# Performance work log

Hardware: AMD Instinct MI355X
Metric: run time of the kernel (lower is better)

Reference implementation:

```python
import jax, jax.numpy as jnp
import numpy as np

V, E, U, B, S = 32000, 512, 1024, 16, 128
BN_EPS = 1e-3  # keras BatchNormalization default


def setup_inputs() -> dict:
    key = jax.random.key(0)
    ks = jax.random.split(key, 12)
    w = 0.05  # small init keeps the relu-activated LSTM recurrence stable
    return {
        "inputs": jax.random.randint(ks[0], (B, S), 0, V),
        "enc_hidden": jax.random.normal(ks[1], (B, U), jnp.float32) * 0.1,
        "enc_cell": jax.random.normal(ks[2], (B, U), jnp.float32) * 0.1,
        "emb": jax.random.normal(ks[3], (V, E), jnp.float32) * w,
        "Wx": jax.random.normal(ks[4], (E, 4 * U), jnp.float32) * w,
        "Wh": jax.random.normal(ks[5], (U, 4 * U), jnp.float32) * w,
        "b": jnp.zeros((4 * U,), jnp.float32),
        "gamma": jnp.ones((U,), jnp.float32),
        "beta": jnp.zeros((U,), jnp.float32),
        "mov_mean": jnp.zeros((U,), jnp.float32),
        "mov_var": jnp.ones((U,), jnp.float32),
        "W1": jax.random.normal(ks[6], (U, U), jnp.float32) * w,
        "b1": jnp.zeros((U,), jnp.float32),
        "W2": jax.random.normal(ks[7], (U, V), jnp.float32) * w,
        "b2": jnp.zeros((V,), jnp.float32),
    }


def _lstm_relu(xg, mask, h0, c0, Wh):
    # xg: [S,B,4U] precomputed input gates; mask: [S,B] (mask_zero semantics)
    def step(carry, inp):
        h, c = carry
        g, m = inp
        z = g + h @ Wh  # [B,4U]
        i, f, cc, o = jnp.split(z, 4, axis=-1)  # keras gate order i,f,c,o
        i = jax.nn.sigmoid(i)
        f = jax.nn.sigmoid(f)
        o = jax.nn.sigmoid(o)
        cc = jax.nn.relu(cc)  # activation='relu' on candidate
        c_new = f * c + i * cc
        h_new = o * jax.nn.relu(c_new)  # activation='relu' on output
        m = m[:, None]
        h_new = jnp.where(m, h_new, h)  # masked step: carry state/output
        c_new = jnp.where(m, c_new, c)
        return (h_new, c_new), h_new

    (_, _), hs = jax.lax.scan(step, (h0, c0), (xg, mask))
    return hs  # [S,B,U]


def reference(inputs, enc_hidden, enc_cell, emb, Wx, Wh, b, gamma, beta,
              mov_mean, mov_var, W1, b1, W2, b2):
    x = emb[inputs]                       # [B,S,E]
    mask = (inputs != 0)                  # mask_zero=True
    xg = jnp.einsum("bse,eg->bsg", x, Wx) + b   # [B,S,4U]
    hs = _lstm_relu(xg.transpose(1, 0, 2), mask.T, enc_hidden, enc_cell, Wh)
    h = hs.transpose(1, 0, 2)             # [B,S,U]
    # BatchNorm (inference: moving statistics), Dropout is identity at inference
    hbn = (h - mov_mean) * jax.lax.rsqrt(mov_var + BN_EPS) * gamma + beta
    d1 = jax.nn.relu(hbn @ W1 + b1)       # [B,S,U]
    logits = d1 @ W2 + b2                 # [B,S,V]
    return jax.nn.softmax(logits, axis=-1)
```

## Files before the change

kernel.cpp:

```cpp
#include <hip/hip_runtime.h>
#include <hip/hip_bf16.h>
#include <stdint.h>

typedef unsigned short u16;
typedef unsigned int u32;
typedef unsigned long long u64;
typedef __attribute__((ext_vector_type(4))) float f32x4;
typedef __attribute__((ext_vector_type(8))) short s16x8;
typedef __attribute__((ext_vector_type(4))) unsigned int u32x4;

#define AT_LD(p)    __hip_atomic_load((p), __ATOMIC_RELAXED, __HIP_MEMORY_SCOPE_AGENT)
#define AT_ST(p, v) __hip_atomic_store((p), (v), __ATOMIC_RELAXED, __HIP_MEMORY_SCOPE_AGENT)
#define AT_FAA(p)   __hip_atomic_fetch_add((p), 1u, __ATOMIC_RELAXED, __HIP_MEMORY_SCOPE_AGENT)


static __device__ __forceinline__ u16 f2bf(float f) {
  union { float f; unsigned u; } v; v.f = f;
  unsigned r = v.u + 0x7FFFu + ((v.u >> 16) & 1u);
  return (u16)(r >> 16);
}

static __device__ __forceinline__ float bf2f(u16 b) {
  union { unsigned u; float f; } v; v.u = ((u32)b) << 16;
  return v.f;
}

static __device__ __forceinline__ void gload_lds16(const void* g, void* l) {
  __builtin_amdgcn_global_load_lds(
      (const __attribute__((address_space(1))) unsigned int*)(uintptr_t)g,
      (__attribute__((address_space(3))) unsigned int*)(uintptr_t)l,
      16, 0, 0);
}

static __device__ __forceinline__ int swzB(int B) {
  int pos = (B >> 4) & 127;
  int row = (B >> 11) & 15;
  int slot = (pos ^ row ^ (pos >> 3)) & 7;
  int npos = (pos & 0x78) | slot;
  return (B & ~0x7F0) | (npos << 4);
}


__global__ void embed_kernel(const int* __restrict__ inputs,
                             const float* __restrict__ emb,
                             u16* __restrict__ xbf) {
  int i = blockIdx.x * 256 + threadIdx.x;
  int row = i >> 6;
  int e0 = (i & 63) << 3;
  int tok = inputs[row];
  const float* src = emb + (size_t)tok * 512 + e0;
  s16x8 o;
#pragma unroll
  for (int j = 0; j < 8; ++j) o[j] = (short)f2bf(src[j]);
  *(s16x8*)(xbf + (size_t)row * 512 + e0) = o;
}

__global__ void mask_kernel(const int* __restrict__ inputs, u64* __restrict__ mb) {
  int t = threadIdx.x;
  if (t < 32) {
    int b = t >> 1, h = t & 1;
    u64 m = 0;
    for (int j = 0; j < 64; ++j)
      m |= (u64)(inputs[b * 128 + h * 64 + j] != 0) << j;
    mb[t] = m;
  }
}

__global__ void transpose_bf16(const float* __restrict__ W, u16* __restrict__ Wt,
                               int K, int N) {
  __shared__ float t[32][33];
  int ntn = N >> 5;
  int tn = blockIdx.x % ntn, tk = blockIdx.x / ntn;
  int n0 = tn << 5, k0 = tk << 5;
  int tx = threadIdx.x & 31, ty = threadIdx.x >> 5;
#pragma unroll
  for (int j = 0; j < 4; ++j) {
    int k = ty * 4 + j;
    t[k][tx] = W[(size_t)(k0 + k) * N + n0 + tx];
  }
  __syncthreads();
#pragma unroll
  for (int j = 0; j < 4; ++j) {
    int n = ty * 4 + j;
    Wt[(size_t)(n0 + n) * K + k0 + tx] = f2bf(t[tx][n]);
  }
}

template <int MODE>
__global__ __launch_bounds__(256)
void gemm_bf16(const u16* __restrict__ A, const u16* __restrict__ Bt,
               const float* __restrict__ bias, void* __restrict__ Cptr,
               float* __restrict__ rowsum, int M, int N, int K) {
  (void)M;
  __shared__ u16 sA[128 * 32];
  __shared__ u16 sB[128 * 32];
  const int nbn = N >> 7;
  const int nwg = gridDim.x;
  int bid = blockIdx.x;
  int q = nwg >> 3;
  int swz = (bid & 7) * q + (bid >> 3);
  int bm = swz / nbn, bn = swz % nbn;
  const int brow = bm << 7, bcol = bn << 7;

  const int tid = threadIdx.x;
  const int lane = tid & 63;
  const int wv = tid >> 6;
  const int wr = (wv >> 1) * 64, wc = (wv & 1) * 64;
  const int ln = lane & 15, kh = lane >> 4;

  const int srow = tid >> 2;
  const int kch = (tid & 3) << 3;

  f32x4 acc[4][4] = {};

  const int nk = K >> 5;
  const u16* Abase = A + (size_t)(brow + srow) * K + kch;
  const u16* Bbase = Bt + (size_t)(bcol + srow) * K + kch;
  const size_t rstride = (size_t)64 * K;
  u16* lA = sA + srow * 32 + kch;
  u16* lB = sB + srow * 32 + kch;

  for (int kt = 0; kt < nk; ++kt) {
    const int k0 = kt << 5;
    gload_lds16(Abase + k0, lA);
    gload_lds16(Abase + rstride + k0, lA + 64 * 32);
    gload_lds16(Bbase + k0, lB);
    gload_lds16(Bbase + rstride + k0, lB + 64 * 32);
    __syncthreads();
    s16x8 aF[4], bF[4];
#pragma unroll
    for (int m = 0; m < 4; ++m)
      aF[m] = *(const s16x8*)(sA + (wr + m * 16 + ln) * 32 + kh * 8);
#pragma unroll
    for (int n = 0; n < 4; ++n)
      bF[n] = *(const s16x8*)(sB + (wc + n * 16 + ln) * 32 + kh * 8);
#pragma unroll
    for (int m = 0; m < 4; ++m)
#pragma unroll
      for (int n = 0; n < 4; ++n)
        acc[m][n] = __builtin_amdgcn_mfma_f32_16x16x32_bf16(aF[m], bF[n], acc[m][n], 0, 0, 0);
    __syncthreads();
  }

  const int browq = brow + wr;
  const int bcolq = bcol + wc;

  if (MODE == 1) {
    u16* O = (u16*)Cptr;
#pragma unroll
    for (int n = 0; n < 4; ++n) {
      int gcol = bcolq + n * 16 + ln;
      float bv = bias[gcol];
#pragma unroll
      for (int m = 0; m < 4; ++m)
#pragma unroll
        for (int r = 0; r < 4; ++r) {
          int grow = browq + m * 16 + kh * 4 + r;
          float v = fmaxf(acc[m][n][r] + bv, 0.f);
          O[(size_t)grow * N + gcol] = f2bf(v);
        }
    }
  } else if (MODE == 3) {
    u16* O = (u16*)Cptr;
    float rs[4][4] = {};
#pragma unroll
    for (int n = 0; n < 4; ++n) {
      int gcol = bcolq + n * 16 + ln;
      float bv = bias[gcol];
#pragma unroll
      for (int m = 0; m < 4; ++m)
#pragma unroll
        for (int r = 0; r < 4; ++r) {
          int grow = browq + m * 16 + kh * 4 + r;
          float v = __expf(acc[m][n][r] + bv);
          rs[m][r] += v;
          O[(size_t)grow * N + gcol] = f2bf(v);
        }
    }
#pragma unroll
    for (int m = 0; m < 4; ++m)
#pragma unroll
      for (int r = 0; r < 4; ++r) {
        float v = rs[m][r];
        v += __shfl_xor(v, 1);
        v += __shfl_xor(v, 2);
        v += __shfl_xor(v, 4);
        v += __shfl_xor(v, 8);
        if (ln == 0) atomicAdd(&rowsum[browq + m * 16 + kh * 4 + r], v);
      }
  } else {
    float* O = (float*)Cptr;
    float rs[4][4] = {};
#pragma unroll
    for (int n = 0; n < 4; ++n) {
      int gcol = bcolq + n * 16 + ln;
      float bv = bias[gcol];
#pragma unroll
      for (int m = 0; m < 4; ++m)
#pragma unroll
        for (int r = 0; r < 4; ++r) {
          int grow = browq + m * 16 + kh * 4 + r;
          float v = acc[m][n][r] + bv;
          if (MODE == 2) { v = __expf(v); rs[m][r] += v; }
          O[(size_t)grow * N + gcol] = v;
        }
    }
    if (MODE == 2) {
#pragma unroll
      for (int m = 0; m < 4; ++m)
#pragma unroll
        for (int r = 0; r < 4; ++r) {
          float v = rs[m][r];
          v += __shfl_xor(v, 1);
          v += __shfl_xor(v, 2);
          v += __shfl_xor(v, 4);
          v += __shfl_xor(v, 8);
          if (ln == 0) atomicAdd(&rowsum[browq + m * 16 + kh * 4 + r], v);
        }
    }
  }
}

__global__ __launch_bounds__(512, 1)
void lstm_kernel(const float* __restrict__ xg,
                 const u16* __restrict__ Wht,
                 const u64* __restrict__ maskb,
                 const float* __restrict__ ench, const float* __restrict__ encc,
                 const float* __restrict__ gamma, const float* __restrict__ beta,
                 const float* __restrict__ mmean, const float* __restrict__ mvar,
                 u32* __restrict__ hbuf32,
                 u16* __restrict__ hbn,
                 u32* __restrict__ cnt) {
  __shared__ char hA[32 * 1024];

  const int wg = blockIdx.x;
  const int u0 = wg << 5;
  const int tid = threadIdx.x;
  const int lane = tid & 63;
  const int wv = tid >> 6;
  const int ln = lane & 15, khq = lane >> 4;

  const int g = ln & 3;
  const int unit = u0 + wv * 4 + (ln >> 2);

  u32x4 bWq[32];
  {
    const u16* wrow = Wht + (size_t)(g * 1024 + unit) * 1024 + khq * 8;
#pragma unroll
    for (int kt = 0; kt < 32; ++kt) {
      const u16* pp = wrow + kt * 32;
      asm volatile("global_load_dwordx4 %0, %1, off" : "=v"(bWq[kt]) : "v"(pp));
    }
    asm volatile("s_waitcnt vmcnt(0)" ::: "memory");
  }

  float cellR[4], holdR[4], xgr[4];
  u64 mA[4], mB[4];
  const float bn_s = gamma[unit] * rsqrtf(mvar[unit] + 1e-3f);
  const float bn_b = beta[unit] - mmean[unit] * bn_s;
  const size_t bstride = (size_t)128 * 4096;
  const float* xbase = xg + (size_t)(khq * 4) * bstride + g * 1024 + unit;
#pragma unroll
  for (int r = 0; r < 4; ++r) {
    int batch = khq * 4 + r;
    cellR[r] = encc[batch * 1024 + unit];
    holdR[r] = ench[batch * 1024 + unit];
    mA[r] = maskb[batch * 2];
    mB[r] = maskb[batch * 2 + 1];
  }
#pragma unroll
  for (int r = 0; r < 4; ++r) {
    u32 w = (u32)f2bf(holdR[r]);
    u32 pw = (u32)__shfl_xor((int)w, 4);
    if ((ln & 7) == 0) {
      int batch = khq * 4 + r;
      AT_ST((u32*)((char*)hbuf32 + batch * 2048 + unit * 2), (w & 0xFFFFu) | (pw << 16));
    }
  }
#pragma unroll
  for (int r = 0; r < 4; ++r) xgr[r] = xbase[r * bstride];
  asm volatile("s_waitcnt vmcnt(0)" ::: "memory");
  __syncthreads();
  if (tid == 0) {
    u32 oldv = AT_FAA(cnt);
    if (oldv != 31u) {
      int c = 0;
      while (AT_LD((const u32*)cnt) < 32u) {
        __builtin_amdgcn_s_sleep(1);
        if (++c > (1 << 18)) break;
      }
    }
  }
  __syncthreads();

  for (int s = 0; s < 128; ++s) {
    u64 st[8];
    {
      const u64* base = (const u64*)((const char*)hbuf32 + (s & 1) * 32768) + tid;
#pragma unroll
      for (int k = 0; k < 8; ++k) {
        const u64* pp = base + k * 512;
        asm volatile("global_load_dwordx2 %0, %1, off sc0 sc1" : "=v"(st[k]) : "v"(pp));
      }
      asm volatile("s_waitcnt vmcnt(0)" ::: "memory");
      __builtin_amdgcn_sched_barrier(0);
#pragma unroll
      for (int k = 0; k < 8; ++k)
        *(u64*)(hA + swzB((tid + k * 512) * 8)) = st[k];
    }
    __syncthreads();

    f32x4 acc0 = {0.f, 0.f, 0.f, 0.f};
    f32x4 acc1 = {0.f, 0.f, 0.f, 0.f};
#pragma unroll
    for (int kt = 0; kt < 32; kt += 2) {
      s16x8 a0 = *(const s16x8*)(hA + swzB(ln * 2048 + kt * 64 + khq * 16));
      acc0 = __builtin_amdgcn_mfma_f32_16x16x32_bf16(
          a0, __builtin_bit_cast(s16x8, bWq[kt]), acc0, 0, 0, 0);
      s16x8 a1 = *(const s16x8*)(hA + swzB(ln * 2048 + (kt + 1) * 64 + khq * 16));
      acc1 = __builtin_amdgcn_mfma_f32_16x16x32_bf16(
          a1, __builtin_bit_cast(s16x8, bWq[kt + 1]), acc1, 0, 0, 0);
    }
    f32x4 accs = acc0 + acc1;

    u32 bnpair[4];
    {
      u16 hbb[4], hbnb[4];
#pragma unroll
      for (int r = 0; r < 4; ++r) {
        float z = accs[r] + xgr[r];
        float sig = 1.f / (1.f + __expf(-z));
        float val = (g == 2) ? fmaxf(z, 0.f) : sig;
        float v1 = __shfl_xor(val, 1);
        float v2 = __shfl_xor(val, 2);
        float v3 = __shfl_xor(val, 3);
        float cnew = v1 * cellR[r] + val * v2;
        float hnew = v3 * fmaxf(cnew, 0.f);
        u64 mm = (s < 64) ? mA[r] : mB[r];
        if (!((mm >> (s & 63)) & 1)) { cnew = cellR[r]; hnew = holdR[r]; }
        cellR[r] = cnew;
        holdR[r] = hnew;
        hbb[r] = f2bf(hnew);
        hbnb[r] = f2bf(hnew * bn_s + bn_b);
      }
#pragma unroll
      for (int r = 0; r < 4; ++r) {
        u32 w = (u32)hbb[r] | ((u32)hbnb[r] << 16);
        u32 pw = (u32)__shfl_xor((int)w, 4);
        u32 hpair = (w & 0xFFFFu) | ((pw & 0xFFFFu) << 16);
        bnpair[r] = (w >> 16) | (pw & 0xFFFF0000u);
        if (s < 127 && (ln & 7) == 0) {
          int batch = khq * 4 + r;
          AT_ST((u32*)((char*)hbuf32 + ((s + 1) & 1) * 32768 + batch * 2048 + unit * 2), hpair);
        }
      }
    }

    if (s < 127) {
      asm volatile("s_waitcnt vmcnt(0)" ::: "memory");
      __syncthreads();
      u32 oldv = 0xFFFFFFFFu;
      if (tid == 0) oldv = AT_FAA(cnt);
      if ((ln & 7) == 0) {
#pragma unroll
        for (int r = 0; r < 4; ++r) {
          int batch = khq * 4 + r;
          *(u32*)((char*)hbn + (size_t)(batch * 128 + s) * 2048 + unit * 2) = bnpair[r];
        }
      }
      {
        const float* xb = xbase + (size_t)(s + 1) * 4096;
#pragma unroll
        for (int r = 0; r < 4; ++r) xgr[r] = xb[r * bstride];
      }
      if (tid == 0) {
        const u32 target = (u32)(s + 2) * 32u;
        if (oldv != target - 1u) {
          int c = 0;
          while (AT_LD((const u32*)cnt) < target) {
            __builtin_amdgcn_s_sleep(1);
            if (++c > (1 << 18)) break;
          }
        }
      }
      __syncthreads();
    } else if ((ln & 7) == 0) {
#pragma unroll
      for (int r = 0; r < 4; ++r) {
        int batch = khq * 4 + r;
        *(u32*)((char*)hbn + (size_t)(batch * 128 + s) * 2048 + unit * 2) = bnpair[r];
      }
    }
  }
}


__global__ void scale_kernel(float* __restrict__ out, const float* __restrict__ rs) {
  const int total4 = 16384000;
  for (int i = blockIdx.x * 256 + threadIdx.x; i < total4; i += gridDim.x * 256) {
    float4* p = (float4*)out + i;
    float4 v = *p;
    int row = i / 8000;
    float sF = 1.0f / rs[row];
    v.x *= sF; v.y *= sF; v.z *= sF; v.w *= sF;
    *p = v;
  }
}

__global__ void scale_bf_kernel(float* __restrict__ out, const u16* __restrict__ e,
                                const float* __restrict__ rs) {
  const int total8 = 8192000;
  for (int i = blockIdx.x * 256 + threadIdx.x; i < total8; i += gridDim.x * 256) {
    s16x8 v = ((const s16x8*)e)[i];
    int row = i / 4000;
    float sF = 1.0f / rs[row];
    float4 o0, o1;
    o0.x = bf2f((u16)v[0]) * sF; o0.y = bf2f((u16)v[1]) * sF;
    o0.z = bf2f((u16)v[2]) * sF; o0.w = bf2f((u16)v[3]) * sF;
    o1.x = bf2f((u16)v[4]) * sF; o1.y = bf2f((u16)v[5]) * sF;
    o1.z = bf2f((u16)v[6]) * sF; o1.w = bf2f((u16)v[7]) * sF;
    ((float4*)out)[2 * i] = o0;
    ((float4*)out)[2 * i + 1] = o1;
  }
}


extern "C" void kernel_launch(void* const* d_in, const int* in_sizes, int n_in,
                              void* d_out, int out_size, void* d_ws, size_t ws_size,
                              hipStream_t stream) {
  (void)in_sizes; (void)n_in; (void)out_size;
  const int*   inputs = (const int*)d_in[0];
  const float* ench   = (const float*)d_in[1];
  const float* encc   = (const float*)d_in[2];
  const float* emb    = (const float*)d_in[3];
  const float* Wx     = (const float*)d_in[4];
  const float* Wh     = (const float*)d_in[5];
  const float* bb     = (const float*)d_in[6];
  const float* gamma  = (const float*)d_in[7];
  const float* beta   = (const float*)d_in[8];
  const float* mmean  = (const float*)d_in[9];
  const float* mvar   = (const float*)d_in[10];
  const float* W1     = (const float*)d_in[11];
  const float* b1     = (const float*)d_in[12];
  const float* W2     = (const float*)d_in[13];
  const float* b2     = (const float*)d_in[14];
  float* out = (float*)d_out;

  char* p = (char*)d_ws;
  u32*   cnt    = (u32*)(p + 0);
  float* rowsum = (float*)(p + 1024);
  u64*   maskb  = (u64*)(p + 10240);
  u32*   hbuf32 = (u32*)(p + 16384);
  size_t off = 81920;
  u16*   xbf  = (u16*)(p + off);     off += (size_t)2048 * 512 * 2;
  u16*   Wxt  = (u16*)(p + off);     off += (size_t)4096 * 512 * 2;
  u16*   Wht  = (u16*)(p + off);     off += (size_t)4096 * 1024 * 2;
  u16*   W1t  = (u16*)(p + off);     off += (size_t)1024 * 1024 * 2;
  u16*   W2t  = (u16*)(p + off);     off += (size_t)32000 * 1024 * 2;
  float* xg   = (float*)(p + off);   off += (size_t)2048 * 4096 * 4;
  u16*   hbn  = (u16*)(p + off);     off += (size_t)2048 * 1024 * 2;
  u16*   d1   = (u16*)(p + off);     off += (size_t)2048 * 1024 * 2;
  size_t off_base = off;
  u16*   expbf = (u16*)(p + off);    off += (size_t)2048 * 32000 * 2;
  if (ws_size < off_base) return;
  const bool bf16path = (ws_size >= off);

  hipMemsetAsync(d_ws, 0, 9216, stream);

  embed_kernel<<<512, 256, 0, stream>>>(inputs, emb, xbf);
  mask_kernel<<<1, 64, 0, stream>>>(inputs, maskb);
  transpose_bf16<<<(512 / 32) * (4096 / 32), 256, 0, stream>>>(Wx, Wxt, 512, 4096);
  transpose_bf16<<<(1024 / 32) * (4096 / 32), 256, 0, stream>>>(Wh, Wht, 1024, 4096);
  transpose_bf16<<<(1024 / 32) * (1024 / 32), 256, 0, stream>>>(W1, W1t, 1024, 1024);
  transpose_bf16<<<(1024 / 32) * (32000 / 32), 256, 0, stream>>>(W2, W2t, 1024, 32000);

  gemm_bf16<0><<<16 * 32, 256, 0, stream>>>(xbf, Wxt, bb, xg, nullptr, 2048, 4096, 512);

  lstm_kernel<<<32, 512, 0, stream>>>(xg, Wht, maskb, ench, encc, gamma, beta,
                                      mmean, mvar, hbuf32, hbn, cnt);

  gemm_bf16<1><<<16 * 8, 256, 0, stream>>>(hbn, W1t, b1, d1, nullptr, 2048, 1024, 1024);

  if (bf16path) {
    gemm_bf16<3><<<16 * 250, 256, 0, stream>>>(d1, W2t, b2, expbf, rowsum, 2048, 32000, 1024);
    scale_bf_kernel<<<2048, 256, 0, stream>>>(out, expbf, rowsum);
  } else {
    gemm_bf16<2><<<16 * 250, 256, 0, stream>>>(d1, W2t, b2, out, rowsum, 2048, 32000, 1024);
    scale_kernel<<<2048, 256, 0, stream>>>(out, rowsum);
  }
}
```

Measured before the change: 962.2 us.

## Use 256x256-tile 4-stage pipelined GEMM for output projection with fused exp

Replaces the 128x128-tile output-projection GEMM (MODE 3) with a dedicated 512-thread kernel using 256x256 tiles, a 4-buffer LDS ring with two stages prefetched ahead, XOR-swizzled LDS layout and MFMA priority hints. The exp, bias and rowsum epilogue is kept. Larger tiles raise arithmetic intensity and halve redundant operand loads for the dominant 2048x32000x1024 GEMM. The cost is 128KB of LDS per block with one block per CU, 1000 workgroups that may leave uneven waves, and higher register pressure from 32 accumulators per thread.

```diff
diff --git a/kernel.cpp b/kernel.cpp
--- a/kernel.cpp
+++ b/kernel.cpp
@@ -160,34 +160,6 @@
           O[(size_t)grow * N + gcol] = f2bf(v);
         }
     }
-  } else if (MODE == 3) {
-    u16* O = (u16*)Cptr;
-    float rs[4][4] = {};
-#pragma unroll
-    for (int n = 0; n < 4; ++n) {
-      int gcol = bcolq + n * 16 + ln;
-      float bv = bias[gcol];
-#pragma unroll
-      for (int m = 0; m < 4; ++m)
-#pragma unroll
-        for (int r = 0; r < 4; ++r) {
-          int grow = browq + m * 16 + kh * 4 + r;
-          float v = __expf(acc[m][n][r] + bv);
-          rs[m][r] += v;
-          O[(size_t)grow * N + gcol] = f2bf(v);
-        }
-    }
-#pragma unroll
-    for (int m = 0; m < 4; ++m)
-#pragma unroll
-      for (int r = 0; r < 4; ++r) {
-        float v = rs[m][r];
-        v += __shfl_xor(v, 1);
-        v += __shfl_xor(v, 2);
-        v += __shfl_xor(v, 4);
-        v += __shfl_xor(v, 8);
-        if (ln == 0) atomicAdd(&rowsum[browq + m * 16 + kh * 4 + r], v);
-      }
   } else {
     float* O = (float*)Cptr;
     float rs[4][4] = {};
@@ -219,6 +191,111 @@
         }
     }
   }
+}
+
+__global__ __launch_bounds__(512, 1)
+void gemm256_exp(const u16* __restrict__ A, const u16* __restrict__ Bt,
+                 const float* __restrict__ bias, u16* __restrict__ O,
+                 float* __restrict__ rowsum, int M, int N, int K) {
+  (void)M;
+  __shared__ char lds[131072];
+  const int nbn = N >> 8;
+  const int nwg = gridDim.x;
+  int bid = blockIdx.x;
+  int q = nwg >> 3;
+  int swz = (bid & 7) * q + (bid >> 3);
+  int bm = swz / nbn, bn = swz % nbn;
+  const int brow = bm << 8, bcol = bn << 8;
+
+  const int tid = threadIdx.x;
+  const int lane = tid & 63;
+  const int wv = tid >> 6;
+  const int wm = wv >> 2, wn = wv & 3;
+  const int ln = lane & 15, kh = lane >> 4;
+
+  const int nk = K >> 5;
+
+  const u16* sbase[4];
+#pragma unroll
+  for (int j = 0; j < 4; ++j) {
+    int cc = (j & 1) * 512 + wv * 64 + lane;
+    int row = cc >> 2, pcol = cc & 3;
+    int lcol = pcol ^ ((row >> 1) & 3);
+    sbase[j] = (j < 2 ? A + (size_t)(brow + row) * K
+                      : Bt + (size_t)(bcol + row) * K) + lcol * 8;
+  }
+
+#define STAGE256(kt, buf)                                                  \
+  {                                                                        \
+    char* lb = lds + (buf) * 32768 + wv * 1024;                            \
+    _Pragma("unroll")                                                      \
+    for (int j = 0; j < 4; ++j)                                            \
+      gload_lds16(sbase[j] + (kt) * 32, lb + j * 8192);                    \
+  }
+
+  f32x4 acc[8][4] = {};
+
+  STAGE256(0, 0);
+  STAGE256(1, 1);
+  asm volatile("s_waitcnt vmcnt(4)" ::: "memory");
+  __syncthreads();
+
+  const char* Ab = lds + (size_t)(wm * 128) * 64;
+  const char* Bb = lds + 16384 + (size_t)(wn * 64) * 64;
+  const int cswz = (kh ^ ((ln >> 1) & 3)) * 16 + ln * 64;
+
+  for (int t = 0; t < nk; ++t) {
+    const int boff = (t & 3) * 32768;
+    if (t + 2 < nk) STAGE256(t + 2, (t + 2) & 3);
+    s16x8 aF[8], bF[4];
+#pragma unroll
+    for (int m = 0; m < 8; ++m)
+      aF[m] = *(const s16x8*)(Ab + boff + m * 1024 + cswz);
+#pragma unroll
+    for (int n = 0; n < 4; ++n)
+      bF[n] = *(const s16x8*)(Bb + boff + n * 1024 + cswz);
+    __builtin_amdgcn_s_setprio(1);
+#pragma unroll
+    for (int m = 0; m < 8; ++m)
+#pragma unroll
+      for (int n = 0; n < 4; ++n)
+        acc[m][n] = __builtin_amdgcn_mfma_f32_16x16x32_bf16(aF[m], bF[n], acc[m][n], 0, 0, 0);
+    __builtin_amdgcn_s_setprio(0);
+    if (t + 2 < nk)
+      asm volatile("s_waitcnt vmcnt(4)" ::: "memory");
+    else
+      asm volatile("s_waitcnt vmcnt(0)" ::: "memory");
+    if (t < nk - 1) __syncthreads();
+  }
+
+  const int browq = brow + wm * 128;
+  const int bcolq = bcol + wn * 64;
+  float rs[8][4] = {};
+#pragma unroll
+  for (int n = 0; n < 4; ++n) {
+    int gcol = bcolq + n * 16 + ln;
+    float bv = bias[gcol];
+#pragma unroll
+    for (int m = 0; m < 8; ++m)
+#pragma unroll
+      for (int r = 0; r < 4; ++r) {
+        float v = __expf(acc[m][n][r] + bv);
+        rs[m][r] += v;
+        O[(size_t)(browq + m * 16 + kh * 4 + r) * N + gcol] = f2bf(v);
+      }
+  }
+#pragma unroll
+  for (int m = 0; m < 8; ++m)
+#pragma unroll
+    for (int r = 0; r < 4; ++r) {
+      float v = rs[m][r];
+      v += __shfl_xor(v, 1);
+      v += __shfl_xor(v, 2);
+      v += __shfl_xor(v, 4);
+      v += __shfl_xor(v, 8);
+      if (ln == 0) atomicAdd(&rowsum[browq + m * 16 + kh * 4 + r], v);
+    }
+#undef STAGE256
 }
 
 __global__ __launch_bounds__(512, 1)
@@ -482,7 +559,7 @@
   gemm_bf16<1><<<16 * 8, 256, 0, stream>>>(hbn, W1t, b1, d1, nullptr, 2048, 1024, 1024);
 
   if (bf16path) {
-    gemm_bf16<3><<<16 * 250, 256, 0, stream>>>(d1, W2t, b2, expbf, rowsum, 2048, 32000, 1024);
+    gemm256_exp<<<8 * 125, 512, 0, stream>>>(d1, W2t, b2, expbf, rowsum, 2048, 32000, 1024);
     scale_bf_kernel<<<2048, 256, 0, stream>>>(out, expbf, rowsum);
   } else {
     gemm_bf16<2><<<16 * 250, 256, 0, stream>>>(d1, W2t, b2, out, rowsum, 2048, 32000, 1024);
```

New measurement: 898.3 us. 1.07x faster.
